# Optimization experiments

Hardware: AMD Instinct MI355X
Metric: run time of the kernel (lower is better)

The kernel has to match this reference:

```python
import jax, jax.numpy as jnp
import numpy as np

B, T, H, LAT, ADIM = 8192, 40, 100, 10, 2
ATT_TEMP = 5.0


def setup_inputs() -> dict:
    key = jax.random.key(0)
    ks = jax.random.split(key, 12)
    return {
        "sampled_att_z": jax.random.normal(ks[0], (B, LAT), jnp.float32),
        "enc_h": jax.random.normal(ks[1], (B, H), jnp.float32),
        # keep IDM params strictly positive / physically plausible to avoid inf
        "idm_params": 1.0 + 2.0 * jax.random.uniform(ks[2], (B, 5), jnp.float32),
        "idm_s": jax.random.uniform(ks[3], (B, T, 8), jnp.float32),
        "sdv_acts": jax.random.normal(ks[4], (B, T, ADIM), jnp.float32),
        "linear_W": jax.random.normal(ks[5], (LAT, H), jnp.float32) / np.float32(np.sqrt(LAT)),
        "linear_b": jnp.zeros((H,), jnp.float32),
        "lstm_Wx": jax.random.normal(ks[6], (H + ADIM, 4 * H), jnp.float32) / np.float32(np.sqrt(H + ADIM)),
        "lstm_Wh": jax.random.normal(ks[7], (H, 4 * H), jnp.float32) / np.float32(np.sqrt(H)),
        "lstm_b": jnp.zeros((4 * H,), jnp.float32),
        "att_W": jax.random.normal(ks[8], (H, 1), jnp.float32) / np.float32(np.sqrt(H)),
        "att_b": jnp.zeros((1,), jnp.float32),
        # precomputed per-step noise, replacing tf.random.normal inside the loop
        "noise_f": jax.random.normal(ks[9], (T, B, 1), jnp.float32),
        "noise_m": jax.random.normal(ks[10], (T, B, 1), jnp.float32),
    }


def reference(sampled_att_z, enc_h, idm_params, idm_s, sdv_acts,
              linear_W, linear_b, lstm_Wx, lstm_Wh, lstm_b, att_W, att_b,
              noise_f, noise_m):
    desired_v = idm_params[:, 0:1]
    desired_tgap = idm_params[:, 1:2]
    min_jamx = idm_params[:, 2:3]
    max_act = idm_params[:, 3:4]
    min_act = idm_params[:, 4:5]

    def idm_driver(vel, dv, dx):  # all [B,1]
        dx = jnp.clip(dx, 0.5, 1000.0)
        desired_gap = min_jamx + jax.nn.relu(
            desired_tgap * vel + vel * dv / (2.0 * jnp.sqrt(max_act * min_act)))
        act = max_act * (1.0 - (vel / desired_v) ** 4 - (desired_gap / dx) ** 2)
        return jnp.clip(act, -3.0, 3.0)

    att_proj = sampled_att_z @ linear_W + linear_b  # [B,H]; also the att_context and init h,c

    s_tm = jnp.swapaxes(idm_s, 0, 1)      # [T,B,8]
    a_tm = jnp.swapaxes(sdv_acts, 0, 1)   # [T,B,ADIM]

    ego_v0 = idm_s[:, 0, 0:1]
    ego_x0 = idm_s[:, 0, 3:4]
    zero_act = jnp.zeros_like(ego_v0)  # step-0 kinematic update is a no-op

    def step(carry, xs):
        ego_v, ego_x, h, c, act = carry
        s, sdv, nf, nm = xs
        ego_v = ego_v + act * 0.1
        ego_x = ego_x + ego_v * 0.1 + 0.5 * act * 0.1 ** 2

        f_v, m_v = s[:, 1:2], s[:, 2:3]
        f_x, m_x = s[:, 4:5], s[:, 5:6]
        f_ex, m_ex = s[:, 6:7], s[:, 7:8]

        ef_act = idm_driver(ego_v, ego_v - f_v, f_x - ego_x)
        ef_act = f_ex * ef_act + (1.0 - f_ex) * nf
        em_act = idm_driver(ego_v, ego_v - m_v, m_x - ego_x)
        em_act = m_ex * em_act + (1.0 - m_ex) * nm

        x_in = jnp.concatenate([att_proj, sdv], axis=-1)  # [B,H+ADIM]
        z = x_in @ lstm_Wx + h @ lstm_Wh + lstm_b          # [B,4H], keras gate order i,f,g,o
        zi, zf, zg, zo = jnp.split(z, 4, axis=-1)
        c = jax.nn.sigmoid(zf) * c + jax.nn.sigmoid(zi) * jnp.tanh(zg)
        h = jax.nn.sigmoid(zo) * jnp.tanh(c)

        att_score = jax.nn.sigmoid(ATT_TEMP * (h @ att_W + att_b))  # [B,1]
        act = (1.0 - att_score) * ef_act + att_score * em_act
        return (ego_v, ego_x, h, c, act), (act, att_score)

    init = (ego_v0, ego_x0, att_proj, att_proj, zero_act)
    _, (acts, atts) = jax.lax.scan(step, init, (s_tm, a_tm, noise_f, noise_m))
    act_seq = jnp.swapaxes(acts, 0, 1)  # [B,T,1]
    att_seq = jnp.swapaxes(atts, 0, 1)  # [B,T,1]
    return act_seq, att_seq
```

## Files before the change

### kernel.cpp

```cpp
#include <hip/hip_runtime.h>
#include <math.h>


#define B_TOT 8192
#define T_STEPS 40
#define NB 16

typedef _Float16 f16;
typedef f16 f16x8 __attribute__((ext_vector_type(8)));
typedef float f32x4 __attribute__((ext_vector_type(4)));

__device__ __forceinline__ float rcpf(float x) { return __builtin_amdgcn_rcpf(x); }
__device__ __forceinline__ float ex2(float x)  { return __builtin_amdgcn_exp2f(x); }
__device__ __forceinline__ float sigf(float x)  { return rcpf(1.f + ex2(-1.44269504f * x)); }
__device__ __forceinline__ float tanhf_(float x){ return fmaf(-2.f, rcpf(1.f + ex2(2.88539008f * x)), 1.f); }


__global__ __launch_bounds__(256) void idm_prep(
    const float* __restrict__ Wx, const float* __restrict__ Wh,
    const float* __restrict__ bvec, const float* __restrict__ attw,
    f16* __restrict__ whb, f16* __restrict__ wxb,
    float* __restrict__ bp)
{
  int i = blockIdx.x * 256 + threadIdx.x;
  int k = i >> 9, n = i & 511;
  int g = n >> 7, j128 = n & 127;
  float vh = 0.f, vx = 0.f;
  if (j128 < 100) {
    int col = g * 100 + j128;
    if (k < 100)      { vh = Wh[k * 400 + col]; vx = Wx[k * 400 + col]; }
    else if (k < 102) { vh = Wx[k * 400 + col]; }
  } else if (n == 100 && k < 100) {
    vh = attw[k];
  }
  int idx = (((n >> 4) * 4 + (k >> 5)) * 64 + (((k >> 3) & 3) * 16 + (n & 15))) * 8 + (k & 7);
  whb[idx] = (f16)vh;
  wxb[idx] = (f16)vx;
  if (i < 512) { int gg = i >> 7, jj = i & 127; bp[i] = (jj < 100) ? bvec[gg * 100 + jj] : 0.f; }
}

#define MM(z, a, g, kf) z = __builtin_amdgcn_mfma_f32_16x16x32_f16(a, wb[g][kf], z, 0, 0, 0)

__global__ __launch_bounds__(512, 4) void idm_main(
    const float* __restrict__ z_att,
    const float* __restrict__ linear_W,
    const float* __restrict__ linear_b,
    const float* __restrict__ sdv_acts,
    const f16* __restrict__ whb, const f16* __restrict__ wxb,
    const float* __restrict__ bp,
    const float* __restrict__ idm_params,
    const float* __restrict__ idm_s,
    const float* __restrict__ att_b,
    const float* __restrict__ noise_f,
    const float* __restrict__ noise_m,
    float* __restrict__ out)
{
  __shared__ f16   hS[2][16][136];
  __shared__ f16   sdvS[T_STEPS][16][2];
  __shared__ float logitS[T_STEPS][16];
  __shared__ float sS[16][T_STEPS][6];
  __shared__ float nS[2][T_STEPS][16];
  __shared__ float accS[2][16][T_STEPS];

  const int tid = threadIdx.x;
  const int w  = tid >> 6;
  const int l  = tid & 63;
  const int lr = l & 15;
  const int lq = l >> 4;
  const int b0g = blockIdx.x * NB;
  const int jcol = 16 * w + lr;

  for (int idx = tid; idx < 2176; idx += 512) ((unsigned*)hS)[idx] = 0u;
  for (int idx = tid; idx < 1280; idx += 512) {
    float v = sdv_acts[(size_t)b0g * 80 + idx];
    int b = idx / 80, r = idx - b * 80;
    sdvS[r >> 1][b][r & 1] = (f16)v;
  }
  for (int idx = tid; idx < 5120; idx += 512) {
    int f = idx & 7;
    if (f != 0 && f != 3) {
      int b = idx / 320, rem = idx - b * 320, t = rem >> 3;
      sS[b][t][(f < 3) ? f - 1 : f - 2] = idm_s[(size_t)b0g * 320 + idx];
    }
  }
  for (int idx = tid; idx < 1280; idx += 512) {
    int which = idx >= 640 ? 1 : 0;
    int r = idx - which * 640;
    int t = r >> 4, i = r & 15;
    nS[which][t][i] = which ? noise_m[(size_t)t * B_TOT + b0g + i]
                            : noise_f[(size_t)t * B_TOT + b0g + i];
  }
  __syncthreads();

  if (tid < 256) {
    int b = tid >> 4, oct = tid & 15;
    float za[10];
    #pragma unroll
    for (int t2 = 0; t2 < 10; ++t2) za[t2] = z_att[(b0g + b) * 10 + t2];
    #pragma unroll
    for (int jj = 0; jj < 8; ++jj) {
      int j = oct * 8 + jj;
      if (j < 100) {
        float acc = linear_b[j];
        #pragma unroll
        for (int t2 = 0; t2 < 10; ++t2) acc = fmaf(za[t2], linear_W[t2 * 100 + j], acc);
        hS[0][b][j] = (f16)acc;
      }
    }
  }
  if (tid < 32) hS[0][tid >> 1][100 + (tid & 1)] = sdvS[0][tid >> 1][tid & 1];
  __syncthreads();

  f16x8 wb[4][4];
  f32x4 cx[4];
  float cst[4];
  if (w < 7) {
    #pragma unroll
    for (int g = 0; g < 4; ++g) {
      int tile = w + 8 * g;
      #pragma unroll
      for (int kf = 0; kf < 4; ++kf)
        wb[g][kf] = *(const f16x8*)(wxb + ((size_t)(tile * 4 + kf) * 64 + l) * 8);
    }
    #pragma unroll
    for (int g = 0; g < 4; ++g) {
      float bpv = bp[(w + 8 * g) * 16 + lr];
      f32x4 c = {bpv, bpv, bpv, bpv};
      cx[g] = c;
    }
    #pragma unroll
    for (int kf = 0; kf < 4; ++kf) {
      f16x8 a = *(const f16x8*)(&hS[0][lr][kf * 32 + lq * 8]);
      #pragma unroll
      for (int g = 0; g < 4; ++g)
        cx[g] = __builtin_amdgcn_mfma_f32_16x16x32_f16(a, wb[g][kf], cx[g], 0, 0, 0);
    }
    #pragma unroll
    for (int g = 0; g < 4; ++g) {
      int tile = w + 8 * g;
      #pragma unroll
      for (int kf = 0; kf < 4; ++kf)
        wb[g][kf] = *(const f16x8*)(whb + ((size_t)(tile * 4 + kf) * 64 + l) * 8);
    }
    #pragma unroll
    for (int r = 0; r < 4; ++r) cst[r] = (float)hS[0][lq * 4 + r][jcol];
  }

  float des_v = 0.f, des_tg = 0.f, min_jx = 0.f, max_a = 0.f;
  float inv2s = 0.f, inv_dv = 0.f, ego_v = 0.f, ego_x = 0.f, attb = 0.f, actT = 0.f;
  if (w == 7 && l < NB) {
    int b = b0g + l;
    const float* P = idm_params + (size_t)b * 5;
    des_v = P[0]; des_tg = P[1]; min_jx = P[2]; max_a = P[3];
    inv2s = 0.5f / sqrtf(max_a * P[4]);
    inv_dv = rcpf(des_v);
    ego_v = idm_s[(size_t)b * 320 + 0];
    ego_x = idm_s[(size_t)b * 320 + 3];
    attb = att_b[0];
    actT = 0.f;
  }

  auto tail_step = [&](int tt) {
    float2 s01 = *(const float2*)&sS[l][tt][0];
    float2 s23 = *(const float2*)&sS[l][tt][2];
    float2 s45 = *(const float2*)&sS[l][tt][4];
    float nf = nS[0][tt][l], nm = nS[1][tt][l];
    float lg = attb + logitS[tt][l];
    ego_v += actT * 0.1f;
    ego_x += ego_v * 0.1f + actT * 0.005f;
    float af_, am_;
    {
      float dx = fminf(fmaxf(s23.x - ego_x, 0.5f), 1000.f);
      float dg = min_jx + fmaxf(0.f, des_tg * ego_v + ego_v * (ego_v - s01.x) * inv2s);
      float r = ego_v * inv_dv; float r2 = r * r; float q = dg * rcpf(dx);
      af_ = fminf(fmaxf(max_a * (1.f - r2 * r2 - q * q), -3.f), 3.f);
    }
    {
      float dx = fminf(fmaxf(s23.y - ego_x, 0.5f), 1000.f);
      float dg = min_jx + fmaxf(0.f, des_tg * ego_v + ego_v * (ego_v - s01.y) * inv2s);
      float r = ego_v * inv_dv; float r2 = r * r; float q = dg * rcpf(dx);
      am_ = fminf(fmaxf(max_a * (1.f - r2 * r2 - q * q), -3.f), 3.f);
    }
    float ef2 = s45.x * af_ + (1.f - s45.x) * nf;
    float em2 = s45.y * am_ + (1.f - s45.y) * nm;
    float att = sigf(5.f * lg);
    actT = (1.f - att) * ef2 + att * em2;
    accS[0][l][tt] = actT;
    accS[1][l][tt] = att;
  };

  int p = 0;
  for (int t = 0; t < T_STEPS; ++t) {
    if (w < 7) {
      f16x8 a0 = *(const f16x8*)(&hS[p][lr][0  + lq * 8]);
      f16x8 a1 = *(const f16x8*)(&hS[p][lr][32 + lq * 8]);
      f16x8 a2 = *(const f16x8*)(&hS[p][lr][64 + lq * 8]);
      f16x8 a3 = *(const f16x8*)(&hS[p][lr][96 + lq * 8]);
      f32x4 z0 = cx[0], z1 = cx[1], z2 = cx[2], z3 = cx[3];
      MM(z0,a0,0,0); MM(z1,a0,1,0); MM(z2,a0,2,0); MM(z3,a0,3,0);
      MM(z0,a1,0,1); MM(z1,a1,1,1); MM(z2,a1,2,1); MM(z3,a1,3,1);
      MM(z0,a2,0,2); MM(z1,a2,1,2); MM(z2,a2,2,2); MM(z3,a2,3,2);
      MM(z0,a3,0,3); MM(z1,a3,1,3); MM(z2,a3,2,3); MM(z3,a3,3,3);

      if (w == 6 && t > 0 && lr == 4) {
        #pragma unroll
        for (int r = 0; r < 4; ++r) logitS[t - 1][lq * 4 + r] = z0[r];
      }

      #pragma unroll
      for (int r = 0; r < 4; ++r) {
        float si = sigf(z0[r]);
        float sf = sigf(z1[r]);
        float tg = tanhf_(z2[r]);
        float so = sigf(z3[r]);
        float cc = fmaf(sf, cst[r], si * tg);
        float hh = so * tanhf_(cc);
        cst[r] = cc;
        if (jcol < 100) hS[p ^ 1][lq * 4 + r][jcol] = (f16)hh;
      }
    } else {
      if (t + 1 < T_STEPS && l < 32)
        hS[p ^ 1][l >> 1][100 + (l & 1)] = sdvS[t + 1][l >> 1][l & 1];
      if (t >= 2 && l < NB) tail_step(t - 2);
    }
    __syncthreads();
    p ^= 1;
  }

  if (w == 6) {
    f32x4 zL = {0.f, 0.f, 0.f, 0.f};
    #pragma unroll
    for (int kf = 0; kf < 4; ++kf) {
      f16x8 a = *(const f16x8*)(&hS[p][lr][kf * 32 + lq * 8]);
      zL = __builtin_amdgcn_mfma_f32_16x16x32_f16(a, wb[0][kf], zL, 0, 0, 0);
    }
    if (lr == 4) {
      #pragma unroll
      for (int r = 0; r < 4; ++r) logitS[T_STEPS - 1][lq * 4 + r] = zL[r];
    }
  }
  if (w == 7 && l < NB) tail_step(T_STEPS - 2);
  __syncthreads();
  if (w == 7 && l < NB) tail_step(T_STEPS - 1);
  __syncthreads();

  if (tid < 160) {
    f32x4 va = ((const f32x4*)&accS[0][0][0])[tid];
    f32x4 vt = ((const f32x4*)&accS[1][0][0])[tid];
    *(f32x4*)(out + (size_t)b0g * T_STEPS + tid * 4) = va;
    *(f32x4*)(out + (size_t)B_TOT * T_STEPS + (size_t)b0g * T_STEPS + tid * 4) = vt;
  }
}

extern "C" void kernel_launch(void* const* d_in, const int* in_sizes, int n_in,
                              void* d_out, int out_size, void* d_ws, size_t ws_size,
                              hipStream_t stream) {
  const float* z_att      = (const float*)d_in[0];
  const float* idm_params = (const float*)d_in[2];
  const float* idm_s      = (const float*)d_in[3];
  const float* sdv_acts   = (const float*)d_in[4];
  const float* linear_W   = (const float*)d_in[5];
  const float* linear_b   = (const float*)d_in[6];
  const float* lstm_Wx    = (const float*)d_in[7];
  const float* lstm_Wh    = (const float*)d_in[8];
  const float* lstm_b     = (const float*)d_in[9];
  const float* att_W      = (const float*)d_in[10];
  const float* att_b      = (const float*)d_in[11];
  const float* noise_f    = (const float*)d_in[12];
  const float* noise_m    = (const float*)d_in[13];
  float* out = (float*)d_out;

  f16*   whb = (f16*)d_ws;
  f16*   wxb = (f16*)((char*)d_ws + 131072);
  float* bp  = (float*)((char*)d_ws + 262144);

  idm_prep<<<256, 256, 0, stream>>>(lstm_Wx, lstm_Wh, lstm_b, att_W, whb, wxb, bp);
  idm_main<<<B_TOT / NB, 512, 0, stream>>>(z_att, linear_W, linear_b, sdv_acts,
                                           whb, wxb, bp,
                                           idm_params, idm_s, att_b,
                                           noise_f, noise_m, out);
}
```

Baseline: 180.3 us.

## Fold exp2 scaling into LSTM weights and merge tail warp into compute warps

The prep kernel now pre-multiplies the LSTM weights and biases by log2(e), or by 2·log2(e) for the tanh gate. The gate activations can then call exp2 directly without a multiply. The dedicated eighth wave that ran the IDM tail and the sdv copy is removed, so the block shrinks to 448 threads. That work now runs on lanes of wave 0 inside the main loop, which is also unrolled by two. This cuts per-step ALU work and a wave per block, but the serial tail step now sits on the critical path of a compute wave before each barrier.

```diff
diff --git a/kernel.cpp b/kernel.cpp
--- a/kernel.cpp
+++ b/kernel.cpp
@@ -25,23 +25,54 @@
   int i = blockIdx.x * 256 + threadIdx.x;
   int k = i >> 9, n = i & 511;
   int g = n >> 7, j128 = n & 127;
+  float sc = (g == 2) ? 2.88539008f : 1.44269504f;
   float vh = 0.f, vx = 0.f;
   if (j128 < 100) {
     int col = g * 100 + j128;
-    if (k < 100)      { vh = Wh[k * 400 + col]; vx = Wx[k * 400 + col]; }
-    else if (k < 102) { vh = Wx[k * 400 + col]; }
+    if (k < 100)      { vh = Wh[k * 400 + col] * sc; vx = Wx[k * 400 + col] * sc; }
+    else if (k < 102) { vh = Wx[k * 400 + col] * sc; }
   } else if (n == 100 && k < 100) {
     vh = attw[k];
   }
   int idx = (((n >> 4) * 4 + (k >> 5)) * 64 + (((k >> 3) & 3) * 16 + (n & 15))) * 8 + (k & 7);
   whb[idx] = (f16)vh;
   wxb[idx] = (f16)vx;
-  if (i < 512) { int gg = i >> 7, jj = i & 127; bp[i] = (jj < 100) ? bvec[gg * 100 + jj] : 0.f; }
+  if (i < 512) {
+    int gg = i >> 7, jj = i & 127;
+    float scb = (gg == 2) ? 2.88539008f : 1.44269504f;
+    bp[i] = (jj < 100) ? bvec[gg * 100 + jj] * scb : 0.f;
+  }
 }
 
 #define MM(z, a, g, kf) z = __builtin_amdgcn_mfma_f32_16x16x32_f16(a, wb[g][kf], z, 0, 0, 0)
 
-__global__ __launch_bounds__(512, 4) void idm_main(
+#define TAIL_STEP(tt) {                                                        \
+    int tt_ = (tt);                                                            \
+    float2 s01 = *(const float2*)&sS[l][tt_][0];                               \
+    float2 s23 = *(const float2*)&sS[l][tt_][2];                               \
+    float2 s45 = *(const float2*)&sS[l][tt_][4];                               \
+    float nf = nS[0][tt_][l], nm = nS[1][tt_][l];                              \
+    float lg = attb + logitS[tt_][l];                                          \
+    ego_v += actT * 0.1f;                                                      \
+    ego_x += ego_v * 0.1f + actT * 0.005f;                                     \
+    float dxf = fminf(fmaxf(s23.x - ego_x, 0.5f), 1000.f);                     \
+    float dgf = min_jx + fmaxf(0.f, des_tg * ego_v + ego_v * (ego_v - s01.x) * inv2s); \
+    float rr = ego_v * inv_dv; float rr2 = rr * rr;                            \
+    float qf = dgf * rcpf(dxf);                                                \
+    float af_ = fminf(fmaxf(max_a * (1.f - rr2 * rr2 - qf * qf), -3.f), 3.f);  \
+    float dxm = fminf(fmaxf(s23.y - ego_x, 0.5f), 1000.f);                     \
+    float dgm = min_jx + fmaxf(0.f, des_tg * ego_v + ego_v * (ego_v - s01.y) * inv2s); \
+    float qm = dgm * rcpf(dxm);                                                \
+    float am_ = fminf(fmaxf(max_a * (1.f - rr2 * rr2 - qm * qm), -3.f), 3.f);  \
+    float ef2 = s45.x * af_ + (1.f - s45.x) * nf;                              \
+    float em2 = s45.y * am_ + (1.f - s45.y) * nm;                              \
+    float att = sigf(5.f * lg);                                                \
+    actT = (1.f - att) * ef2 + att * em2;                                      \
+    accS[0][l][tt_] = actT;                                                    \
+    accS[1][l][tt_] = att;                                                     \
+  }
+
+__global__ __launch_bounds__(448, 4) void idm_main(
     const float* __restrict__ z_att,
     const float* __restrict__ linear_W,
     const float* __restrict__ linear_b,
@@ -69,21 +100,22 @@
   const int lq = l >> 4;
   const int b0g = blockIdx.x * NB;
   const int jcol = 16 * w + lr;
-
-  for (int idx = tid; idx < 2176; idx += 512) ((unsigned*)hS)[idx] = 0u;
-  for (int idx = tid; idx < 1280; idx += 512) {
+  const bool tail_lane = (tid < NB);
+
+  for (int idx = tid; idx < 2176; idx += 448) ((unsigned*)hS)[idx] = 0u;
+  for (int idx = tid; idx < 1280; idx += 448) {
     float v = sdv_acts[(size_t)b0g * 80 + idx];
     int b = idx / 80, r = idx - b * 80;
     sdvS[r >> 1][b][r & 1] = (f16)v;
   }
-  for (int idx = tid; idx < 5120; idx += 512) {
+  for (int idx = tid; idx < 5120; idx += 448) {
     int f = idx & 7;
     if (f != 0 && f != 3) {
       int b = idx / 320, rem = idx - b * 320, t = rem >> 3;
       sS[b][t][(f < 3) ? f - 1 : f - 2] = idm_s[(size_t)b0g * 320 + idx];
     }
   }
-  for (int idx = tid; idx < 1280; idx += 512) {
+  for (int idx = tid; idx < 1280; idx += 448) {
     int which = idx >= 640 ? 1 : 0;
     int r = idx - which * 640;
     int t = r >> 4, i = r & 15;
@@ -112,43 +144,42 @@
   __syncthreads();
 
   f16x8 wb[4][4];
+  #pragma unroll
+  for (int g = 0; g < 4; ++g) {
+    int tile = w + 8 * g;
+    #pragma unroll
+    for (int kf = 0; kf < 4; ++kf)
+      wb[g][kf] = *(const f16x8*)(wxb + ((size_t)(tile * 4 + kf) * 64 + l) * 8);
+  }
   f32x4 cx[4];
+  #pragma unroll
+  for (int g = 0; g < 4; ++g) {
+    float bpv = bp[(w + 8 * g) * 16 + lr];
+    f32x4 c = {bpv, bpv, bpv, bpv};
+    cx[g] = c;
+  }
+  #pragma unroll
+  for (int kf = 0; kf < 4; ++kf) {
+    f16x8 a = *(const f16x8*)(&hS[0][lr][kf * 32 + lq * 8]);
+    #pragma unroll
+    for (int g = 0; g < 4; ++g)
+      cx[g] = __builtin_amdgcn_mfma_f32_16x16x32_f16(a, wb[g][kf], cx[g], 0, 0, 0);
+  }
+  #pragma unroll
+  for (int g = 0; g < 4; ++g) {
+    int tile = w + 8 * g;
+    #pragma unroll
+    for (int kf = 0; kf < 4; ++kf)
+      wb[g][kf] = *(const f16x8*)(whb + ((size_t)(tile * 4 + kf) * 64 + l) * 8);
+  }
+
   float cst[4];
-  if (w < 7) {
-    #pragma unroll
-    for (int g = 0; g < 4; ++g) {
-      int tile = w + 8 * g;
-      #pragma unroll
-      for (int kf = 0; kf < 4; ++kf)
-        wb[g][kf] = *(const f16x8*)(wxb + ((size_t)(tile * 4 + kf) * 64 + l) * 8);
-    }
-    #pragma unroll
-    for (int g = 0; g < 4; ++g) {
-      float bpv = bp[(w + 8 * g) * 16 + lr];
-      f32x4 c = {bpv, bpv, bpv, bpv};
-      cx[g] = c;
-    }
-    #pragma unroll
-    for (int kf = 0; kf < 4; ++kf) {
-      f16x8 a = *(const f16x8*)(&hS[0][lr][kf * 32 + lq * 8]);
-      #pragma unroll
-      for (int g = 0; g < 4; ++g)
-        cx[g] = __builtin_amdgcn_mfma_f32_16x16x32_f16(a, wb[g][kf], cx[g], 0, 0, 0);
-    }
-    #pragma unroll
-    for (int g = 0; g < 4; ++g) {
-      int tile = w + 8 * g;
-      #pragma unroll
-      for (int kf = 0; kf < 4; ++kf)
-        wb[g][kf] = *(const f16x8*)(whb + ((size_t)(tile * 4 + kf) * 64 + l) * 8);
-    }
-    #pragma unroll
-    for (int r = 0; r < 4; ++r) cst[r] = (float)hS[0][lq * 4 + r][jcol];
-  }
-
-  float des_v = 0.f, des_tg = 0.f, min_jx = 0.f, max_a = 0.f;
-  float inv2s = 0.f, inv_dv = 0.f, ego_v = 0.f, ego_x = 0.f, attb = 0.f, actT = 0.f;
-  if (w == 7 && l < NB) {
+  #pragma unroll
+  for (int r = 0; r < 4; ++r) cst[r] = (float)hS[0][lq * 4 + r][jcol];
+
+  float des_v = 1.f, des_tg = 0.f, min_jx = 0.f, max_a = 1.f;
+  float inv2s = 0.f, inv_dv = 1.f, ego_v = 0.f, ego_x = 0.f, attb = 0.f, actT = 0.f;
+  if (tail_lane) {
     int b = b0g + l;
     const float* P = idm_params + (size_t)b * 5;
     des_v = P[0]; des_tg = P[1]; min_jx = P[2]; max_a = P[3];
@@ -157,72 +188,40 @@
     ego_v = idm_s[(size_t)b * 320 + 0];
     ego_x = idm_s[(size_t)b * 320 + 3];
     attb = att_b[0];
-    actT = 0.f;
-  }
-
-  auto tail_step = [&](int tt) {
-    float2 s01 = *(const float2*)&sS[l][tt][0];
-    float2 s23 = *(const float2*)&sS[l][tt][2];
-    float2 s45 = *(const float2*)&sS[l][tt][4];
-    float nf = nS[0][tt][l], nm = nS[1][tt][l];
-    float lg = attb + logitS[tt][l];
-    ego_v += actT * 0.1f;
-    ego_x += ego_v * 0.1f + actT * 0.005f;
-    float af_, am_;
-    {
-      float dx = fminf(fmaxf(s23.x - ego_x, 0.5f), 1000.f);
-      float dg = min_jx + fmaxf(0.f, des_tg * ego_v + ego_v * (ego_v - s01.x) * inv2s);
-      float r = ego_v * inv_dv; float r2 = r * r; float q = dg * rcpf(dx);
-      af_ = fminf(fmaxf(max_a * (1.f - r2 * r2 - q * q), -3.f), 3.f);
-    }
-    {
-      float dx = fminf(fmaxf(s23.y - ego_x, 0.5f), 1000.f);
-      float dg = min_jx + fmaxf(0.f, des_tg * ego_v + ego_v * (ego_v - s01.y) * inv2s);
-      float r = ego_v * inv_dv; float r2 = r * r; float q = dg * rcpf(dx);
-      am_ = fminf(fmaxf(max_a * (1.f - r2 * r2 - q * q), -3.f), 3.f);
-    }
-    float ef2 = s45.x * af_ + (1.f - s45.x) * nf;
-    float em2 = s45.y * am_ + (1.f - s45.y) * nm;
-    float att = sigf(5.f * lg);
-    actT = (1.f - att) * ef2 + att * em2;
-    accS[0][l][tt] = actT;
-    accS[1][l][tt] = att;
-  };
+  }
 
   int p = 0;
+  #pragma unroll 2
   for (int t = 0; t < T_STEPS; ++t) {
-    if (w < 7) {
-      f16x8 a0 = *(const f16x8*)(&hS[p][lr][0  + lq * 8]);
-      f16x8 a1 = *(const f16x8*)(&hS[p][lr][32 + lq * 8]);
-      f16x8 a2 = *(const f16x8*)(&hS[p][lr][64 + lq * 8]);
-      f16x8 a3 = *(const f16x8*)(&hS[p][lr][96 + lq * 8]);
-      f32x4 z0 = cx[0], z1 = cx[1], z2 = cx[2], z3 = cx[3];
-      MM(z0,a0,0,0); MM(z1,a0,1,0); MM(z2,a0,2,0); MM(z3,a0,3,0);
-      MM(z0,a1,0,1); MM(z1,a1,1,1); MM(z2,a1,2,1); MM(z3,a1,3,1);
-      MM(z0,a2,0,2); MM(z1,a2,1,2); MM(z2,a2,2,2); MM(z3,a2,3,2);
-      MM(z0,a3,0,3); MM(z1,a3,1,3); MM(z2,a3,2,3); MM(z3,a3,3,3);
-
-      if (w == 6 && t > 0 && lr == 4) {
-        #pragma unroll
-        for (int r = 0; r < 4; ++r) logitS[t - 1][lq * 4 + r] = z0[r];
-      }
-
+    f16x8 a0 = *(const f16x8*)(&hS[p][lr][0  + lq * 8]);
+    f16x8 a1 = *(const f16x8*)(&hS[p][lr][32 + lq * 8]);
+    f16x8 a2 = *(const f16x8*)(&hS[p][lr][64 + lq * 8]);
+    f16x8 a3 = *(const f16x8*)(&hS[p][lr][96 + lq * 8]);
+    f32x4 z0 = cx[0], z1 = cx[1], z2 = cx[2], z3 = cx[3];
+    MM(z0,a0,0,0); MM(z1,a0,1,0); MM(z2,a0,2,0); MM(z3,a0,3,0);
+    MM(z0,a1,0,1); MM(z1,a1,1,1); MM(z2,a1,2,1); MM(z3,a1,3,1);
+    MM(z0,a2,0,2); MM(z1,a2,1,2); MM(z2,a2,2,2); MM(z3,a2,3,2);
+    MM(z0,a3,0,3); MM(z1,a3,1,3); MM(z2,a3,2,3); MM(z3,a3,3,3);
+
+    if (w == 6 && t > 0 && lr == 4) {
       #pragma unroll
-      for (int r = 0; r < 4; ++r) {
-        float si = sigf(z0[r]);
-        float sf = sigf(z1[r]);
-        float tg = tanhf_(z2[r]);
-        float so = sigf(z3[r]);
-        float cc = fmaf(sf, cst[r], si * tg);
-        float hh = so * tanhf_(cc);
-        cst[r] = cc;
-        if (jcol < 100) hS[p ^ 1][lq * 4 + r][jcol] = (f16)hh;
-      }
-    } else {
-      if (t + 1 < T_STEPS && l < 32)
-        hS[p ^ 1][l >> 1][100 + (l & 1)] = sdvS[t + 1][l >> 1][l & 1];
-      if (t >= 2 && l < NB) tail_step(t - 2);
-    }
+      for (int r = 0; r < 4; ++r) logitS[t - 1][lq * 4 + r] = z0[r];
+    }
+
+    #pragma unroll
+    for (int r = 0; r < 4; ++r) {
+      float si = rcpf(1.f + ex2(-z0[r]));
+      float sf = rcpf(1.f + ex2(-z1[r]));
+      float tg = fmaf(-2.f, rcpf(1.f + ex2(z2[r])), 1.f);
+      float so = rcpf(1.f + ex2(-z3[r]));
+      float cc = fmaf(sf, cst[r], si * tg);
+      float hh = so * tanhf_(cc);
+      cst[r] = cc;
+      if (jcol < 100) hS[p ^ 1][lq * 4 + r][jcol] = (f16)hh;
+    }
+    if (t + 1 < T_STEPS && tid < 32)
+      hS[p ^ 1][tid >> 1][100 + (tid & 1)] = sdvS[t + 1][tid >> 1][tid & 1];
+    if (tail_lane && t >= 2) TAIL_STEP(t - 2);
     __syncthreads();
     p ^= 1;
   }
@@ -239,9 +238,9 @@
       for (int r = 0; r < 4; ++r) logitS[T_STEPS - 1][lq * 4 + r] = zL[r];
     }
   }
-  if (w == 7 && l < NB) tail_step(T_STEPS - 2);
-  __syncthreads();
-  if (w == 7 && l < NB) tail_step(T_STEPS - 1);
+  if (tail_lane) TAIL_STEP(T_STEPS - 2);
+  __syncthreads();
+  if (tail_lane) TAIL_STEP(T_STEPS - 1);
   __syncthreads();
 
   if (tid < 160) {
@@ -275,7 +274,7 @@
   float* bp  = (float*)((char*)d_ws + 262144);
 
   idm_prep<<<256, 256, 0, stream>>>(lstm_Wx, lstm_Wh, lstm_b, att_W, whb, wxb, bp);
-  idm_main<<<B_TOT / NB, 512, 0, stream>>>(z_att, linear_W, linear_b, sdv_acts,
+  idm_main<<<B_TOT / NB, 448, 0, stream>>>(z_att, linear_W, linear_b, sdv_acts,
                                            whb, wxb, bp,
                                            idm_params, idm_s, att_b,
                                            noise_f, noise_m, out);
```

New measurement: 178.5 us. Within noise of the previous version (-1.0%).
